# Performance work log

Measured on AMD Instinct MI355X. Metric: run time of the kernel, lower is better.

Reference implementation:

```python
import jax, jax.numpy as jnp
import numpy as np

DIM = 32     # per-head dim in LiteMLA
EPS = 1e-15


def _conv(x, w, groups=1, padding=0, bias=None):
    out = jax.lax.conv_general_dilated(
        x, w, window_strides=(1, 1),
        padding=[(padding, padding), (padding, padding)],
        dimension_numbers=('NCHW', 'OIHW', 'NCHW'),
        feature_group_count=groups)
    if bias is not None:
        out = out + bias[None, :, None, None]
    return out


def _bn(x, g, b):
    # inference-mode BatchNorm2d with running_mean=0, running_var=1
    return x * g[None, :, None, None] + b[None, :, None, None]


def _hswish(x):
    return x * jnp.clip(x + 3.0, 0.0, 6.0) * (1.0 / 6.0)


def _relu_linear_att(kv, q):
    # kv: (B, h*2*DIM, H, W), q: (B, h*DIM, H, W)
    B, _, H, W = kv.shape
    kvr = kv.reshape(B, -1, 2 * DIM, H * W).transpose(0, 1, 3, 2)  # (B,h,HW,2d)
    qr = q.reshape(B, -1, DIM, H * W).transpose(0, 1, 3, 2)        # (B,h,HW,d)
    k = jax.nn.relu(kvr[..., :DIM])
    v = kvr[..., DIM:]
    qf = jax.nn.relu(qr)
    # pad v with a ones column (denominator trick)
    vpad = jnp.pad(v, ((0, 0), (0, 0), (0, 0), (0, 1)), constant_values=1.0)
    ctx = jnp.einsum('bhnd,bhne->bhde', k, vpad)   # (B,h,d,d+1)
    out = jnp.einsum('bhnd,bhde->bhne', qf, ctx)   # (B,h,HW,d+1)
    out = out[..., :-1] / (out[..., -1:] + EPS)
    return out.transpose(0, 1, 3, 2).reshape(B, -1, H, W)


def setup_inputs() -> dict:
    key = jax.random.key(0)
    ks = iter(jax.random.split(key, 40))
    C, B, H, W = 256, 4, 64, 64
    heads = C // DIM  # 8; total_dim = heads*DIM = C

    def rn(shape, s=0.05):
        return jax.random.normal(next(ks), shape, jnp.float32) * s

    inp = {
        'rgb': jax.random.normal(next(ks), (B, C, H, W), jnp.float32),
        't': jax.random.normal(next(ks), (B, C, H, W), jnp.float32),
        # MBConv1: in=2C, mid=round(2C*0.5)=C, out=C, all bn2d, hswish/hswish/None
        'm1_inv_w': rn((C, 2 * C, 1, 1)), 'm1_inv_g': 1.0 + rn((C,)), 'm1_inv_b': rn((C,)),
        'm1_dw_w': rn((C, 1, 3, 3)), 'm1_dw_g': 1.0 + rn((C,)), 'm1_dw_b': rn((C,)),
        'm1_pw_w': rn((C, C, 1, 1)), 'm1_pw_g': 1.0 + rn((C,)), 'm1_pw_b': rn((C,)),
        # LiteMLA projections (1x1, no bias/norm/act)
        'kv_w': rn((4 * C, C, 1, 1)),
        'qrgb_w': rn((C, C, 1, 1)),
        'qt_w': rn((C, C, 1, 1)),
        # multi-scale aggregation (scale=5): depthwise 5x5 then grouped 1x1
        'agg_kv_dw': rn((4 * C, 1, 5, 5)), 'agg_kv_pw': rn((4 * C, DIM, 1, 1)),  # groups=4*heads
        'agg_t_dw': rn((C, 1, 5, 5)), 'agg_t_pw': rn((C, DIM, 1, 1)),            # groups=heads
        'agg_rgb_dw': rn((C, 1, 5, 5)), 'agg_rgb_pw': rn((C, DIM, 1, 1)),
        # proj: 1x1, 2*total_dim*(1+len(scales)) = 4C -> C, no bias, norm 'hswish' unregistered -> None
        'proj_w': rn((C, 4 * C, 1, 1)),
        # MBConv2: mid=4C, use_bias=(T,T,F), norm=(None,None,bn2d), act=(hswish,hswish,None)
        'm2_inv_w': rn((4 * C, C, 1, 1)), 'm2_inv_bias': rn((4 * C,)),
        'm2_dw_w': rn((4 * C, 1, 3, 3)), 'm2_dw_bias': rn((4 * C,)),
        'm2_pw_w': rn((C, 4 * C, 1, 1)), 'm2_pw_g': 1.0 + rn((C,)), 'm2_pw_b': rn((C,)),
    }
    return inp


def reference(rgb, t, m1_inv_w, m1_inv_g, m1_inv_b, m1_dw_w, m1_dw_g, m1_dw_b,
              m1_pw_w, m1_pw_g, m1_pw_b, kv_w, qrgb_w, qt_w,
              agg_kv_dw, agg_kv_pw, agg_t_dw, agg_t_pw, agg_rgb_dw, agg_rgb_pw,
              proj_w, m2_inv_w, m2_inv_bias, m2_dw_w, m2_dw_bias,
              m2_pw_w, m2_pw_g, m2_pw_b):
    C = rgb.shape[1]
    heads = C // DIM
    # MBConv1 on cat(rgb, t)
    x = jnp.concatenate([rgb, t], axis=1)
    x = _hswish(_bn(_conv(x, m1_inv_w), m1_inv_g, m1_inv_b))
    x = _hswish(_bn(_conv(x, m1_dw_w, groups=C, padding=1), m1_dw_g, m1_dw_b))
    rgbt = _bn(_conv(x, m1_pw_w), m1_pw_g, m1_pw_b)
    # LiteMLA
    kv = _conv(rgbt, kv_w)          # (B,4C,H,W)
    q_t = _conv(t, qt_w)            # (B,C,H,W)
    q_rgb = _conv(rgb, qrgb_w)
    kv_s = _conv(_conv(kv, agg_kv_dw, groups=4 * C, padding=2), agg_kv_pw, groups=4 * heads)
    qt_s = _conv(_conv(q_t, agg_t_dw, groups=C, padding=2), agg_t_pw, groups=heads)
    qrgb_s = _conv(_conv(q_rgb, agg_rgb_dw, groups=C, padding=2), agg_rgb_pw, groups=heads)
    kv1 = jnp.concatenate([kv[:, :2 * C], kv_s[:, :2 * C]], axis=1)   # (B,4C,H,W)
    kv2 = jnp.concatenate([kv[:, 2 * C:], kv_s[:, 2 * C:]], axis=1)
    mq_t = jnp.concatenate([q_t, qt_s], axis=1)                       # (B,2C,H,W)
    mq_rgb = jnp.concatenate([q_rgb, qrgb_s], axis=1)
    out1 = _relu_linear_att(kv1, mq_t)
    out2 = _relu_linear_att(kv2, mq_rgb)
    out = _conv(jnp.concatenate([out1, out2], axis=1), proj_w)        # (B,C,H,W)
    # MBConv2
    x = _hswish(_conv(out, m2_inv_w, bias=m2_inv_bias))
    x = _hswish(_conv(x, m2_dw_w, groups=4 * C, padding=1, bias=m2_dw_bias))
    x = _bn(_conv(x, m2_pw_w), m2_pw_g, m2_pw_b)
    return x
```

## Files before the change

kernel.cpp:

```cpp
#include <hip/hip_runtime.h>

#define HW 4096
#define S_E ((size_t)4 * 256 * 4096)

using f16   = _Float16;
using f16x8 = __attribute__((ext_vector_type(8))) _Float16;
using f32x4 = __attribute__((ext_vector_type(4))) float;

__device__ __forceinline__ float hswish(float x) {
  float r = fminf(fmaxf(x + 3.0f, 0.0f), 6.0f);
  return x * r * (1.0f / 6.0f);
}

__device__ __forceinline__ void atomic_add_f32(float* p, float v) {
  __hip_atomic_fetch_add(p, v, __ATOMIC_RELAXED, __HIP_MEMORY_SCOPE_AGENT);
}

__global__ __launch_bounds__(256) void zero_buf4(float4* __restrict__ p, int n4) {
  int i = blockIdx.x * 256 + threadIdx.x;
  if (i < n4) p[i] = make_float4(0.f, 0.f, 0.f, 0.f);
}

__global__ __launch_bounds__(256) void cvt_planes(
    const float* __restrict__ in, f16* __restrict__ hi, f16* __restrict__ lo, int n4)
{
  int i = blockIdx.x * 256 + threadIdx.x;
  if (i >= n4) return;
  float4 v = ((const float4*)in)[i];
  const float* f = &v.x;
  unsigned int hw[2], lw[2];
  #pragma unroll
  for (int j = 0; j < 2; ++j) {
    f16 h0 = (f16)f[2 * j], h1 = (f16)f[2 * j + 1];
    f16 l0 = (f16)(f[2 * j] - (float)h0), l1 = (f16)(f[2 * j + 1] - (float)h1);
    hw[j] = (unsigned int)__builtin_bit_cast(unsigned short, h0) |
            ((unsigned int)__builtin_bit_cast(unsigned short, h1) << 16);
    lw[j] = (unsigned int)__builtin_bit_cast(unsigned short, l0) |
            ((unsigned int)__builtin_bit_cast(unsigned short, l1) << 16);
  }
  *(uint2*)(hi + 4 * (size_t)i) = make_uint2(hw[0], hw[1]);
  *(uint2*)(lo + 4 * (size_t)i) = make_uint2(lw[0], lw[1]);
}

__global__ __launch_bounds__(256) void gemm_mfma(
    const f16* __restrict__ xhi0, const f16* __restrict__ xlo0,
    const f16* __restrict__ xhi1, const f16* __restrict__ xlo1,
    const f16* __restrict__ whi, const f16* __restrict__ wlo,
    float* __restrict__ out, f16* __restrict__ ohi, f16* __restrict__ olo,
    const float* __restrict__ scale, const float* __restrict__ bias,
    int K, int k0, int CO, int epi)
{
  __shared__ f16 Bh[64 * 36];
  __shared__ f16 Bl[64 * 36];
  const int p0  = blockIdx.x * 64;
  const int co0 = blockIdx.y * 128;
  const int b   = blockIdx.z;
  const int tid = threadIdx.x;
  const int lane = tid & 63;
  const int wave = tid >> 6;
  const int wc = wave & 1, wp = wave >> 1;
  const int k1 = K - k0;

  const int tt    = tid & 127;
  const int kbase = (tt >> 3) * 2;
  const int poct  = (tt & 7) * 8;
  const f16* x0 = (tid < 128) ? xhi0 : xlo0;
  const f16* x1 = (tid < 128) ? xhi1 : xlo1;
  f16* Bp = (tid < 128) ? Bh : Bl;

  const int q  = lane >> 4;
  const int ln = lane & 15;

  f32x4 acc[4][2];
  #pragma unroll
  for (int im = 0; im < 4; ++im)
    #pragma unroll
    for (int in = 0; in < 2; ++in)
      acc[im][in] = (f32x4){0.f, 0.f, 0.f, 0.f};

  uint4 g0, g1;
  {
    int kg = kbase;
    const f16* x = (kg < k0) ? x0 + ((size_t)b * k0 + kg) * HW
                             : x1 + ((size_t)b * k1 + (kg - k0)) * HW;
    g0 = *(const uint4*)(x + p0 + poct);
    g1 = *(const uint4*)(x + HW + p0 + poct);
  }

  for (int kt = 0; kt < K; kt += 32) {
    {
      const unsigned short* u0 = (const unsigned short*)&g0;
      const unsigned short* u1 = (const unsigned short*)&g1;
      #pragma unroll
      for (int i = 0; i < 8; ++i) {
        unsigned int d = (unsigned int)u0[i] | ((unsigned int)u1[i] << 16);
        *(unsigned int*)(Bp + (poct + i) * 36 + kbase) = d;
      }
    }
    __syncthreads();
    if (kt + 32 < K) {
      int kg = kt + 32 + kbase;
      const f16* x = (kg < k0) ? x0 + ((size_t)b * k0 + kg) * HW
                               : x1 + ((size_t)b * k1 + (kg - k0)) * HW;
      g0 = *(const uint4*)(x + p0 + poct);
      g1 = *(const uint4*)(x + HW + p0 + poct);
    }
    f16x8 bh[2], bl[2];
    #pragma unroll
    for (int in = 0; in < 2; ++in) {
      const f16* fp = &Bh[(wp * 32 + in * 16 + ln) * 36 + q * 8];
      const f16* gp = &Bl[(wp * 32 + in * 16 + ln) * 36 + q * 8];
      ((uint2*)&bh[in])[0] = *(const uint2*)fp;
      ((uint2*)&bh[in])[1] = *(const uint2*)(fp + 4);
      ((uint2*)&bl[in])[0] = *(const uint2*)gp;
      ((uint2*)&bl[in])[1] = *(const uint2*)(gp + 4);
    }
    #pragma unroll
    for (int im = 0; im < 4; ++im) {
      size_t wofs = (size_t)(co0 + wc * 64 + im * 16 + ln) * K + kt + q * 8;
      f16x8 ah = *(const f16x8*)(whi + wofs);
      f16x8 al = *(const f16x8*)(wlo + wofs);
      #pragma unroll
      for (int in = 0; in < 2; ++in) {
        acc[im][in] = __builtin_amdgcn_mfma_f32_16x16x32_f16(ah, bh[in], acc[im][in], 0, 0, 0);
        acc[im][in] = __builtin_amdgcn_mfma_f32_16x16x32_f16(ah, bl[in], acc[im][in], 0, 0, 0);
        acc[im][in] = __builtin_amdgcn_mfma_f32_16x16x32_f16(al, bh[in], acc[im][in], 0, 0, 0);
      }
    }
    __syncthreads();
  }

  #pragma unroll
  for (int im = 0; im < 4; ++im) {
    #pragma unroll
    for (int in = 0; in < 2; ++in) {
      int p = p0 + wp * 32 + in * 16 + ln;
      #pragma unroll
      for (int r = 0; r < 4; ++r) {
        int co = co0 + wc * 64 + im * 16 + q * 4 + r;
        float v = acc[im][in][r];
        if (epi == 1)      v = v * scale[co] + bias[co];
        else if (epi == 2) v = hswish(v * scale[co] + bias[co]);
        else if (epi == 3) v = hswish(v + bias[co]);
        size_t idx = ((size_t)b * CO + co) * HW + p;
        if (out) out[idx] = v;
        else {
          f16 h = (f16)v;
          ohi[idx] = h;
          olo[idx] = (f16)(v - (float)h);
        }
      }
    }
  }
}

__global__ __launch_bounds__(256) void dwconv3(
    const float* __restrict__ in, const float* __restrict__ w,
    float* __restrict__ out, f16* __restrict__ ohi, f16* __restrict__ olo,
    const float* __restrict__ scale, const float* __restrict__ bias,
    int Cmask, int epi, int pmode)
{
  __shared__ float tl[66 * 66];
  const int bc = blockIdx.x;
  const int c  = bc & Cmask;
  const float* src = in + (size_t)bc * HW;
  const int t = threadIdx.x;
  for (int i = t; i < 66 * 66; i += 256) {
    int r = i / 66, cc = i - r * 66;
    int gy = r - 1, gx = cc - 1;
    float v = 0.0f;
    if (gy >= 0 && gy < 64 && gx >= 0 && gx < 64) v = src[(gy << 6) + gx];
    tl[i] = v;
  }
  const float* wp = w + c * 9;
  float w00 = wp[0], w01 = wp[1], w02 = wp[2];
  float w10 = wp[3], w11 = wp[4], w12 = wp[5];
  float w20 = wp[6], w21 = wp[7], w22 = wp[8];
  float g = (epi == 2) ? scale[c] : 1.0f;
  float bb = bias[c];
  __syncthreads();
  #pragma unroll 4
  for (int j = 0; j < 16; ++j) {
    int p = j * 256 + t;
    int y = p >> 6, x = p & 63;
    const float* bp = &tl[y * 66 + x];
    float s;
    s = w00 * bp[0]        + w01 * bp[1]        + w02 * bp[2];
    s = fmaf(w10, bp[66],    fmaf(w11, bp[67],    fmaf(w12, bp[68],  s)));
    s = fmaf(w20, bp[132],   fmaf(w21, bp[133],   fmaf(w22, bp[134], s)));
    float v = (epi == 2) ? hswish(s * g + bb) : hswish(s + bb);
    size_t idx = (size_t)bc * HW + p;
    if (pmode) {
      f16 h = (f16)v;
      ohi[idx] = h;
      olo[idx] = (f16)(v - (float)h);
    } else {
      out[idx] = v;
    }
  }
}

__global__ __launch_bounds__(256) void agg_fused(
    const float* __restrict__ in, const float* __restrict__ dw,
    const float* __restrict__ pw, float* __restrict__ out, int C)
{
  __shared__ float in_t[16 * 12 * 68];
  __shared__ float dww[32 * 25];
  __shared__ float pww[32 * 32];
  const int g = blockIdx.x, b = blockIdx.y, tile = blockIdx.z;
  const int t = threadIdx.x;
  const int y0 = tile * 8;
  const float* src = in + ((size_t)b * C + g * 32) * HW;

  for (int i = t; i < 800; i += 256)  dww[i] = dw[(size_t)g * 800 + i];
  for (int i = t; i < 1024; i += 256) pww[i] = pw[(size_t)g * 1024 + i];

  const int x = t & 63, yl = t >> 6;
  float acca[32] = {}, accb[32] = {};

  for (int ph = 0; ph < 2; ++ph) {
    __syncthreads();
    #pragma unroll
    for (int i = 0; i < 12; ++i) {
      int id = i * 256 + t;
      int qq = id & 15;
      int rid = id >> 4;
      int ch = rid / 12, r = rid - ch * 12;
      int gy = y0 - 2 + r;
      float4 v = make_float4(0.f, 0.f, 0.f, 0.f);
      if (gy >= 0 && gy < 64)
        v = *(const float4*)(src + (size_t)(ph * 16 + ch) * HW + (gy << 6) + (qq << 2));
      *(float4*)&in_t[(ch * 12 + r) * 68 + 2 + (qq << 2)] = v;
    }
    #pragma unroll
    for (int i = 0; i < 3; ++i) {
      int id = i * 256 + t;
      int side = id & 3;
      int rid = id >> 2;
      int col = (side < 2) ? side : 64 + side;
      in_t[rid * 68 + col] = 0.0f;
    }
    __syncthreads();
    for (int cl = 0; cl < 16; ++cl) {
      int ci = ph * 16 + cl;
      const float* bp = &in_t[(cl * 12) * 68 + 2 + x];
      const float* wv = &dww[ci * 25];
      float da = 0.f, db = 0.f;
      #pragma unroll
      for (int k = 0; k < 25; ++k) {
        int dy = k / 5, dx = (k % 5) - 2;
        float w = wv[k];
        da = fmaf(w, bp[(yl + dy) * 68 + dx], da);
        db = fmaf(w, bp[(yl + 4 + dy) * 68 + dx], db);
      }
      #pragma unroll
      for (int m = 0; m < 32; ++m) {
        float w = pww[m * 32 + ci];
        acca[m] = fmaf(w, da, acca[m]);
        accb[m] = fmaf(w, db, accb[m]);
      }
    }
  }
  float* dst = out + ((size_t)b * C + g * 32) * HW + y0 * 64;
  #pragma unroll
  for (int m = 0; m < 32; ++m) {
    dst[(size_t)m * HW + (yl << 6) + x]        = acca[m];
    dst[(size_t)m * HW + ((yl + 4) << 6) + x]  = accb[m];
  }
}

__global__ __launch_bounds__(256) void att_ctx(
    const float* __restrict__ kv, const float* __restrict__ kvs,
    float* __restrict__ ctxbuf)
{
  __shared__ float tile[64 * 128];
  __shared__ float red[4 * 1056];
  const int head  = blockIdx.x;
  const int b     = blockIdx.y;
  const int slice = blockIdx.z & 31;
  const int z     = blockIdx.z >> 5;
  const int tid   = threadIdx.x;
  const int lane  = tid & 63;
  const int wave  = tid >> 6;
  const int td = lane & 7, te = lane >> 3;

  const float* kvsrc = (head < 8)
      ? kv  + ((size_t)b * 1024 + z * 512 + head * 64) * HW
      : kvs + ((size_t)b * 1024 + z * 512 + (head - 8) * 64) * HW;
  const int n0 = slice * 128;

  #pragma unroll
  for (int j = 0; j < 8; ++j) {
    int slot = j * 256 + tid;
    int ch = slot >> 5;
    int nb = slot & 31;
    float4 v = *(const float4*)(kvsrc + (size_t)ch * HW + n0 + (nb << 2));
    if (ch < 32) {
      v.x = fmaxf(v.x, 0.0f); v.y = fmaxf(v.y, 0.0f);
      v.z = fmaxf(v.z, 0.0f); v.w = fmaxf(v.w, 0.0f);
    }
    int sw = nb ^ ((ch >> 2) & 7);
    *(float4*)&tile[ch * 128 + (sw << 2)] = v;
  }
  __syncthreads();

  float acc[4][4] = {};
  float cs[4] = {};
  #pragma unroll
  for (int j = 0; j < 8; ++j) {
    int nblk = wave * 8 + j;
    float4 kr[4], vr[4];
    #pragma unroll
    for (int r = 0; r < 4; ++r) {
      int d = td * 4 + r;
      kr[r] = *(const float4*)&tile[d * 128 + ((nblk ^ td) << 2)];
      int e = 32 + te * 4 + r;
      vr[r] = *(const float4*)&tile[e * 128 + ((nblk ^ te) << 2)];
    }
    #pragma unroll
    for (int r = 0; r < 4; ++r) {
      const float* kp = &kr[r].x;
      cs[r] += kp[0] + kp[1] + kp[2] + kp[3];
      #pragma unroll
      for (int rp = 0; rp < 4; ++rp) {
        const float* vp = &vr[rp].x;
        acc[r][rp] = fmaf(kp[0], vp[0],
                     fmaf(kp[1], vp[1],
                     fmaf(kp[2], vp[2],
                     fmaf(kp[3], vp[3], acc[r][rp]))));
      }
    }
  }

  float* rw = &red[wave * 1056];
  #pragma unroll
  for (int r = 0; r < 4; ++r) {
    #pragma unroll
    for (int rp = 0; rp < 4; ++rp)
      rw[(td * 4 + r) * 33 + te * 4 + rp] = acc[r][rp];
    if (te == 0) rw[(td * 4 + r) * 33 + 32] = cs[r];
  }
  __syncthreads();

  float* cp = ctxbuf + (size_t)(((z * 4 + b) * 16) + head) * 1056;
  for (int i = tid; i < 1056; i += 256) {
    float s = red[i] + red[1056 + i] + red[2112 + i] + red[3168 + i];
    atomic_add_f32(cp + i, s);
  }
}

__global__ __launch_bounds__(256) void att_apply(
    const float* __restrict__ ctxbuf,
    const float* __restrict__ q0, const float* __restrict__ q0s,
    const float* __restrict__ q1, const float* __restrict__ q1s,
    f16* __restrict__ H)
{
  __shared__ float ctx[1056];
  const int head = blockIdx.x;
  const int b    = blockIdx.y;
  const int tile = blockIdx.z & 15;
  const int z    = blockIdx.z >> 4;
  const int tid  = threadIdx.x;

  const float* cp = ctxbuf + (size_t)(((z * 4 + b) * 16) + head) * 1056;
  for (int i = tid; i < 1056; i += 256) ctx[i] = cp[i];
  __syncthreads();

  const float* qb = (z == 0) ? (head < 8 ? q0 : q0s) : (head < 8 ? q1 : q1s);
  const float* qsrc = qb + ((size_t)b * 256 + (head & 7) * 32) * HW;
  f16* oh = H + (size_t)z * (4 * S_E);
  f16* ol = oh + 2 * S_E;

  const int n = tile * 256 + tid;
  float qv[32];
  #pragma unroll
  for (int d = 0; d < 32; ++d)
    qv[d] = fmaxf(qsrc[(size_t)d * HW + n], 0.0f);
  float den = 1e-15f;
  #pragma unroll
  for (int d = 0; d < 32; ++d)
    den = fmaf(qv[d], ctx[d * 33 + 32], den);
  float rden = 1.0f / den;
  for (int e = 0; e < 32; ++e) {
    float s = 0.0f;
    #pragma unroll
    for (int d = 0; d < 32; ++d)
      s = fmaf(qv[d], ctx[d * 33 + e], s);
    float v = s * rden;
    size_t idx = ((size_t)b * 512 + head * 32 + e) * HW + n;
    f16 h = (f16)v;
    oh[idx] = h;
    ol[idx] = (f16)(v - (float)h);
  }
}

extern "C" void kernel_launch(void* const* d_in, const int* in_sizes, int n_in,
                              void* d_out, int out_size, void* d_ws, size_t ws_size,
                              hipStream_t stream) {
  (void)in_sizes; (void)n_in; (void)out_size; (void)ws_size;
  const float* rgb         = (const float*)d_in[0];
  const float* t           = (const float*)d_in[1];
  const float* m1_inv_w    = (const float*)d_in[2];
  const float* m1_inv_g    = (const float*)d_in[3];
  const float* m1_inv_b    = (const float*)d_in[4];
  const float* m1_dw_w     = (const float*)d_in[5];
  const float* m1_dw_g     = (const float*)d_in[6];
  const float* m1_dw_b     = (const float*)d_in[7];
  const float* m1_pw_w     = (const float*)d_in[8];
  const float* m1_pw_g     = (const float*)d_in[9];
  const float* m1_pw_b     = (const float*)d_in[10];
  const float* kv_w        = (const float*)d_in[11];
  const float* qrgb_w      = (const float*)d_in[12];
  const float* qt_w        = (const float*)d_in[13];
  const float* agg_kv_dw   = (const float*)d_in[14];
  const float* agg_kv_pw   = (const float*)d_in[15];
  const float* agg_t_dw    = (const float*)d_in[16];
  const float* agg_t_pw    = (const float*)d_in[17];
  const float* agg_rgb_dw  = (const float*)d_in[18];
  const float* agg_rgb_pw  = (const float*)d_in[19];
  const float* proj_w      = (const float*)d_in[20];
  const float* m2_inv_w    = (const float*)d_in[21];
  const float* m2_inv_bias = (const float*)d_in[22];
  const float* m2_dw_w     = (const float*)d_in[23];
  const float* m2_dw_bias  = (const float*)d_in[24];
  const float* m2_pw_w     = (const float*)d_in[25];
  const float* m2_pw_g     = (const float*)d_in[26];
  const float* m2_pw_b     = (const float*)d_in[27];
  float* outp = (float*)d_out;

  const size_t S = S_E;
  float* ws = (float*)d_ws;
  f16*   rgbH  = (f16*)(ws + 0 * S);
  f16*   tH    = (f16*)(ws + 1 * S);
  float* s2    = ws + 2 * S;
  f16*   dw1H  = (f16*)(ws + 3 * S);
  float* s3f   = ws + 3 * S;
  f16*   rgbtH = (f16*)(ws + 4 * S);
  float* s4f   = ws + 4 * S;
  float* s5    = ws + 5 * S;
  float* KV    = ws + 6 * S;
  f16*   attH  = (f16*)(ws + 6 * S);
  float* KVS   = ws + 10 * S;
  float* CTX   = ws + 14 * S;
  float* WB    = ws + 14 * S + 150016;
  f16*   projH = (f16*)(ws + 15 * S);

  f16* wb = (f16*)WB;
  f16* w_m1inv = wb;
  f16* w_m1pw  = wb + 262144;
  f16* w_kv    = wb + 393216;
  f16* w_qt    = wb + 917504;
  f16* w_qrgb  = wb + 1048576;
  f16* w_proj  = wb + 1179648;
  f16* w_m2inv = wb + 1703936;
  f16* w_m2pw  = wb + 2228224;

  dim3 blk(256);
  const int XN4 = (int)(S_E / 4);

  cvt_planes<<<dim3(4096), blk, 0, stream>>>(rgb, rgbH, rgbH + S_E, XN4);
  cvt_planes<<<dim3(4096), blk, 0, stream>>>(t,   tH,   tH   + S_E, XN4);
  cvt_planes<<<dim3(128), blk, 0, stream>>>(m1_inv_w, w_m1inv, w_m1inv + 131072, 32768);
  cvt_planes<<<dim3(64),  blk, 0, stream>>>(m1_pw_w,  w_m1pw,  w_m1pw  + 65536, 16384);
  cvt_planes<<<dim3(256), blk, 0, stream>>>(kv_w,     w_kv,    w_kv    + 262144, 65536);
  cvt_planes<<<dim3(64),  blk, 0, stream>>>(qt_w,     w_qt,    w_qt    + 65536, 16384);
  cvt_planes<<<dim3(64),  blk, 0, stream>>>(qrgb_w,   w_qrgb,  w_qrgb  + 65536, 16384);
  cvt_planes<<<dim3(256), blk, 0, stream>>>(proj_w,   w_proj,  w_proj  + 262144, 65536);
  cvt_planes<<<dim3(256), blk, 0, stream>>>(m2_inv_w, w_m2inv, w_m2inv + 262144, 65536);
  cvt_planes<<<dim3(256), blk, 0, stream>>>(m2_pw_w,  w_m2pw,  w_m2pw  + 262144, 65536);

  gemm_mfma<<<dim3(64, 2, 4), blk, 0, stream>>>(
      rgbH, rgbH + S_E, tH, tH + S_E, w_m1inv, w_m1inv + 131072,
      s2, nullptr, nullptr, m1_inv_g, m1_inv_b, 512, 256, 256, 2);
  dwconv3<<<dim3(1024), blk, 0, stream>>>(
      s2, m1_dw_w, nullptr, dw1H, dw1H + S_E, m1_dw_g, m1_dw_b, 255, 2, 1);
  gemm_mfma<<<dim3(64, 2, 4), blk, 0, stream>>>(
      dw1H, dw1H + S_E, dw1H, dw1H + S_E, w_m1pw, w_m1pw + 65536,
      nullptr, rgbtH, rgbtH + S_E, m1_pw_g, m1_pw_b, 256, 256, 256, 1);

  gemm_mfma<<<dim3(64, 8, 4), blk, 0, stream>>>(
      rgbtH, rgbtH + S_E, rgbtH, rgbtH + S_E, w_kv, w_kv + 262144,
      KV, nullptr, nullptr, nullptr, nullptr, 256, 256, 1024, 0);
  gemm_mfma<<<dim3(64, 2, 4), blk, 0, stream>>>(
      tH, tH + S_E, tH, tH + S_E, w_qt, w_qt + 65536,
      s2, nullptr, nullptr, nullptr, nullptr, 256, 256, 256, 0);
  gemm_mfma<<<dim3(64, 2, 4), blk, 0, stream>>>(
      rgbH, rgbH + S_E, rgbH, rgbH + S_E, w_qrgb, w_qrgb + 65536,
      s5, nullptr, nullptr, nullptr, nullptr, 256, 256, 256, 0);

  agg_fused<<<dim3(32, 4, 8), blk, 0, stream>>>(KV, agg_kv_dw, agg_kv_pw, KVS, 1024);
  agg_fused<<<dim3(8, 4, 8),  blk, 0, stream>>>(s2, agg_t_dw,  agg_t_pw,  s3f, 256);
  agg_fused<<<dim3(8, 4, 8),  blk, 0, stream>>>(s5, agg_rgb_dw, agg_rgb_pw, s4f, 256);

  zero_buf4<<<dim3(132), blk, 0, stream>>>((float4*)CTX, 128 * 264);
  att_ctx<<<dim3(16, 4, 64), blk, 0, stream>>>(KV, KVS, CTX);
  att_apply<<<dim3(16, 4, 32), blk, 0, stream>>>(CTX, s2, s3f, s5, s4f, attH);

  gemm_mfma<<<dim3(64, 2, 4), blk, 0, stream>>>(
      attH, attH + 2 * S_E, attH + 4 * S_E, attH + 6 * S_E, w_proj, w_proj + 262144,
      nullptr, projH, projH + S_E, nullptr, nullptr, 1024, 512, 256, 0);
  gemm_mfma<<<dim3(64, 8, 4), blk, 0, stream>>>(
      projH, projH + S_E, projH, projH + S_E, w_m2inv, w_m2inv + 262144,
      KVS, nullptr, nullptr, nullptr, m2_inv_bias, 256, 256, 1024, 3);
  dwconv3<<<dim3(4096), blk, 0, stream>>>(
      KVS, m2_dw_w, nullptr, (f16*)(ws + 6 * S), (f16*)(ws + 8 * S),
      nullptr, m2_dw_bias, 1023, 3, 1);
  gemm_mfma<<<dim3(64, 2, 4), blk, 0, stream>>>(
      (f16*)(ws + 6 * S), (f16*)(ws + 8 * S), (f16*)(ws + 6 * S), (f16*)(ws + 8 * S),
      w_m2pw, w_m2pw + 262144,
      outp, nullptr, nullptr, m2_pw_g, m2_pw_b, 1024, 1024, 256, 1);
}
```

Baseline: 845.2 us.

## Double-buffer LDS tiles in MFMA GEMM with two-stage global prefetch

New measurement: 885.5 us. 1.05x slower.

```diff
diff --git a/kernel.cpp b/kernel.cpp
--- a/kernel.cpp
+++ b/kernel.cpp
@@ -6,6 +6,8 @@
 using f16   = _Float16;
 using f16x8 = __attribute__((ext_vector_type(8))) _Float16;
 using f32x4 = __attribute__((ext_vector_type(4))) float;
+
+template<int N> struct IC { static constexpr int v = N; };
 
 __device__ __forceinline__ float hswish(float x) {
   float r = fminf(fmaxf(x + 3.0f, 0.0f), 6.0f);
@@ -50,8 +52,8 @@
     const float* __restrict__ scale, const float* __restrict__ bias,
     int K, int k0, int CO, int epi)
 {
-  __shared__ f16 Bh[64 * 36];
-  __shared__ f16 Bl[64 * 36];
+  __shared__ f16 Bh[2][64 * 36];
+  __shared__ f16 Bl[2][64 * 36];
   const int p0  = blockIdx.x * 64;
   const int co0 = blockIdx.y * 128;
   const int b   = blockIdx.z;
@@ -66,7 +68,8 @@
   const int poct  = (tt & 7) * 8;
   const f16* x0 = (tid < 128) ? xhi0 : xlo0;
   const f16* x1 = (tid < 128) ? xhi1 : xlo1;
-  f16* Bp = (tid < 128) ? Bh : Bl;
+  f16* Bp0 = (tid < 128) ? Bh[0] : Bl[0];
+  f16* Bp1 = (tid < 128) ? Bh[1] : Bl[1];
 
   const int q  = lane >> 4;
   const int ln = lane & 15;
@@ -78,56 +81,91 @@
     for (int in = 0; in < 2; ++in)
       acc[im][in] = (f32x4){0.f, 0.f, 0.f, 0.f};
 
-  uint4 g0, g1;
+  auto gaddr = [&](int kg) -> const f16* {
+    return (kg < k0) ? x0 + ((size_t)b * k0 + kg) * HW
+                     : x1 + ((size_t)b * k1 + (kg - k0)) * HW;
+  };
+
+  uint4 gA0, gA1, gB0, gB1;
   {
-    int kg = kbase;
-    const f16* x = (kg < k0) ? x0 + ((size_t)b * k0 + kg) * HW
-                             : x1 + ((size_t)b * k1 + (kg - k0)) * HW;
-    g0 = *(const uint4*)(x + p0 + poct);
-    g1 = *(const uint4*)(x + HW + p0 + poct);
-  }
-
-  for (int kt = 0; kt < K; kt += 32) {
-    {
-      const unsigned short* u0 = (const unsigned short*)&g0;
-      const unsigned short* u1 = (const unsigned short*)&g1;
-      #pragma unroll
-      for (int i = 0; i < 8; ++i) {
-        unsigned int d = (unsigned int)u0[i] | ((unsigned int)u1[i] << 16);
-        *(unsigned int*)(Bp + (poct + i) * 36 + kbase) = d;
-      }
-    }
-    __syncthreads();
-    if (kt + 32 < K) {
-      int kg = kt + 32 + kbase;
-      const f16* x = (kg < k0) ? x0 + ((size_t)b * k0 + kg) * HW
-                               : x1 + ((size_t)b * k1 + (kg - k0)) * HW;
-      g0 = *(const uint4*)(x + p0 + poct);
-      g1 = *(const uint4*)(x + HW + p0 + poct);
+    const f16* x = gaddr(kbase);
+    gA0 = *(const uint4*)(x + p0 + poct);
+    gA1 = *(const uint4*)(x + HW + p0 + poct);
+  }
+  {
+    const unsigned short* u0 = (const unsigned short*)&gA0;
+    const unsigned short* u1 = (const unsigned short*)&gA1;
+    #pragma unroll
+    for (int i = 0; i < 8; ++i) {
+      unsigned int d = (unsigned int)u0[i] | ((unsigned int)u1[i] << 16);
+      *(unsigned int*)(Bp0 + (poct + i) * 36 + kbase) = d;
+    }
+  }
+  {
+    const f16* x = gaddr(32 + kbase);
+    gB0 = *(const uint4*)(x + p0 + poct);
+    gB1 = *(const uint4*)(x + HW + p0 + poct);
+  }
+  __builtin_amdgcn_sched_barrier(0);
+  asm volatile("s_waitcnt lgkmcnt(0)" ::: "memory");
+  __builtin_amdgcn_s_barrier();
+  __builtin_amdgcn_sched_barrier(0);
+
+  auto subiter = [&](auto Sc, int kt) {
+    constexpr int S = decltype(Sc)::v;
+    const int kk = kt + S * 32;
+    f16x8 wh[4], wl[4];
+    #pragma unroll
+    for (int im = 0; im < 4; ++im) {
+      size_t wofs = (size_t)(co0 + wc * 64 + im * 16 + ln) * K + kk + q * 8;
+      wh[im] = *(const f16x8*)(whi + wofs);
+      wl[im] = *(const f16x8*)(wlo + wofs);
     }
     f16x8 bh[2], bl[2];
     #pragma unroll
     for (int in = 0; in < 2; ++in) {
-      const f16* fp = &Bh[(wp * 32 + in * 16 + ln) * 36 + q * 8];
-      const f16* gp = &Bl[(wp * 32 + in * 16 + ln) * 36 + q * 8];
+      const f16* fp = &Bh[S][(wp * 32 + in * 16 + ln) * 36 + q * 8];
+      const f16* gp = &Bl[S][(wp * 32 + in * 16 + ln) * 36 + q * 8];
       ((uint2*)&bh[in])[0] = *(const uint2*)fp;
       ((uint2*)&bh[in])[1] = *(const uint2*)(fp + 4);
       ((uint2*)&bl[in])[0] = *(const uint2*)gp;
       ((uint2*)&bl[in])[1] = *(const uint2*)(gp + 4);
     }
+    if (kk + 64 < K) {
+      const f16* x = gaddr(kk + 64 + kbase);
+      if (S) { gB0 = *(const uint4*)(x + p0 + poct); gB1 = *(const uint4*)(x + HW + p0 + poct); }
+      else   { gA0 = *(const uint4*)(x + p0 + poct); gA1 = *(const uint4*)(x + HW + p0 + poct); }
+    }
     #pragma unroll
     for (int im = 0; im < 4; ++im) {
-      size_t wofs = (size_t)(co0 + wc * 64 + im * 16 + ln) * K + kt + q * 8;
-      f16x8 ah = *(const f16x8*)(whi + wofs);
-      f16x8 al = *(const f16x8*)(wlo + wofs);
       #pragma unroll
       for (int in = 0; in < 2; ++in) {
-        acc[im][in] = __builtin_amdgcn_mfma_f32_16x16x32_f16(ah, bh[in], acc[im][in], 0, 0, 0);
-        acc[im][in] = __builtin_amdgcn_mfma_f32_16x16x32_f16(ah, bl[in], acc[im][in], 0, 0, 0);
-        acc[im][in] = __builtin_amdgcn_mfma_f32_16x16x32_f16(al, bh[in], acc[im][in], 0, 0, 0);
+        acc[im][in] = __builtin_amdgcn_mfma_f32_16x16x32_f16(wh[im], bh[in], acc[im][in], 0, 0, 0);
+        acc[im][in] = __builtin_amdgcn_mfma_f32_16x16x32_f16(wh[im], bl[in], acc[im][in], 0, 0, 0);
+        acc[im][in] = __builtin_amdgcn_mfma_f32_16x16x32_f16(wl[im], bh[in], acc[im][in], 0, 0, 0);
       }
     }
-    __syncthreads();
+    if (kk + 32 < K) {
+      f16* Bw = S ? Bp0 : Bp1;
+      const uint4 h0 = S ? gA0 : gB0;
+      const uint4 h1 = S ? gA1 : gB1;
+      const unsigned short* u0 = (const unsigned short*)&h0;
+      const unsigned short* u1 = (const unsigned short*)&h1;
+      #pragma unroll
+      for (int i = 0; i < 8; ++i) {
+        unsigned int d = (unsigned int)u0[i] | ((unsigned int)u1[i] << 16);
+        *(unsigned int*)(Bw + (poct + i) * 36 + kbase) = d;
+      }
+      __builtin_amdgcn_sched_barrier(0);
+      asm volatile("s_waitcnt lgkmcnt(0)" ::: "memory");
+      __builtin_amdgcn_s_barrier();
+      __builtin_amdgcn_sched_barrier(0);
+    }
+  };
+
+  for (int kt = 0; kt < K; kt += 64) {
+    subiter(IC<0>{}, kt);
+    subiter(IC<1>{}, kt);
   }
 
   #pragma unroll
```

## Emit transposed packed hi/lo activations and stream them directly into MFMA GEMMs

Applied to the files above, without the earlier changes.

New measurement: 912.5 us. +8.0%, slower.

```diff
diff --git a/kernel.cpp b/kernel.cpp
--- a/kernel.cpp
+++ b/kernel.cpp
@@ -6,6 +6,7 @@
 using f16   = _Float16;
 using f16x8 = __attribute__((ext_vector_type(8))) _Float16;
 using f32x4 = __attribute__((ext_vector_type(4))) float;
+using u32x4 = __attribute__((ext_vector_type(4))) unsigned int;
 
 __device__ __forceinline__ float hswish(float x) {
   float r = fminf(fmaxf(x + 3.0f, 0.0f), 6.0f);
@@ -47,6 +48,7 @@
     const f16* __restrict__ xhi1, const f16* __restrict__ xlo1,
     const f16* __restrict__ whi, const f16* __restrict__ wlo,
     float* __restrict__ out, f16* __restrict__ ohi, f16* __restrict__ olo,
+    unsigned int* __restrict__ oxt,
     const float* __restrict__ scale, const float* __restrict__ bias,
     int K, int k0, int CO, int epi)
 {
@@ -135,6 +137,119 @@
     #pragma unroll
     for (int in = 0; in < 2; ++in) {
       int p = p0 + wp * 32 + in * 16 + ln;
+      if (oxt) {
+        unsigned int pk[4];
+        #pragma unroll
+        for (int r = 0; r < 4; ++r) {
+          int co = co0 + wc * 64 + im * 16 + q * 4 + r;
+          float v = acc[im][in][r];
+          if (epi == 1)      v = v * scale[co] + bias[co];
+          else if (epi == 2) v = hswish(v * scale[co] + bias[co]);
+          else if (epi == 3) v = hswish(v + bias[co]);
+          f16 h = (f16)v;
+          f16 l = (f16)(v - (float)h);
+          pk[r] = ((unsigned int)__builtin_bit_cast(unsigned short, h) << 16) |
+                   (unsigned int)__builtin_bit_cast(unsigned short, l);
+        }
+        int cob = co0 + wc * 64 + im * 16 + q * 4;
+        *(uint4*)(oxt + ((size_t)b * HW + p) * CO + cob) =
+            make_uint4(pk[0], pk[1], pk[2], pk[3]);
+      } else {
+        #pragma unroll
+        for (int r = 0; r < 4; ++r) {
+          int co = co0 + wc * 64 + im * 16 + q * 4 + r;
+          float v = acc[im][in][r];
+          if (epi == 1)      v = v * scale[co] + bias[co];
+          else if (epi == 2) v = hswish(v * scale[co] + bias[co]);
+          else if (epi == 3) v = hswish(v + bias[co]);
+          size_t idx = ((size_t)b * CO + co) * HW + p;
+          if (out) out[idx] = v;
+          else {
+            f16 h = (f16)v;
+            ohi[idx] = h;
+            olo[idx] = (f16)(v - (float)h);
+          }
+        }
+      }
+    }
+  }
+}
+
+__global__ __launch_bounds__(256) void gemm_stream(
+    const unsigned int* __restrict__ XT,
+    const f16* __restrict__ whi, const f16* __restrict__ wlo,
+    float* __restrict__ out,
+    const float* __restrict__ scale, const float* __restrict__ bias,
+    int K, int CO, int epi)
+{
+  const int p0  = blockIdx.x * 64;
+  const int co0 = blockIdx.y * 128;
+  const int b   = blockIdx.z;
+  const int tid = threadIdx.x;
+  const int lane = tid & 63;
+  const int wave = tid >> 6;
+  const int wc = wave & 1, wp = wave >> 1;
+  const int q  = lane >> 4;
+  const int ln = lane & 15;
+
+  const unsigned int* xb = XT + (size_t)b * HW * K;
+
+  f32x4 acc[4][2];
+  #pragma unroll
+  for (int im = 0; im < 4; ++im)
+    #pragma unroll
+    for (int in = 0; in < 2; ++in)
+      acc[im][in] = (f32x4){0.f, 0.f, 0.f, 0.f};
+
+  #pragma unroll 2
+  for (int kt = 0; kt < K; kt += 32) {
+    u32x4 a[2], c[2];
+    #pragma unroll
+    for (int in = 0; in < 2; ++in) {
+      int p = p0 + wp * 32 + in * 16 + ln;
+      const unsigned int* src = xb + (size_t)p * K + kt + q * 8;
+      a[in] = *(const u32x4*)src;
+      c[in] = *(const u32x4*)(src + 4);
+    }
+    f16x8 wh[4], wl[4];
+    #pragma unroll
+    for (int im = 0; im < 4; ++im) {
+      size_t wofs = (size_t)(co0 + wc * 64 + im * 16 + ln) * K + kt + q * 8;
+      wh[im] = *(const f16x8*)(whi + wofs);
+      wl[im] = *(const f16x8*)(wlo + wofs);
+    }
+    f16x8 bh[2], bl[2];
+    #pragma unroll
+    for (int in = 0; in < 2; ++in) {
+      u32x4 hh, ll;
+      hh.x = (a[in].x >> 16) | (a[in].y & 0xffff0000u);
+      hh.y = (a[in].z >> 16) | (a[in].w & 0xffff0000u);
+      hh.z = (c[in].x >> 16) | (c[in].y & 0xffff0000u);
+      hh.w = (c[in].z >> 16) | (c[in].w & 0xffff0000u);
+      ll.x = (a[in].x & 0xffffu) | (a[in].y << 16);
+      ll.y = (a[in].z & 0xffffu) | (a[in].w << 16);
+      ll.z = (c[in].x & 0xffffu) | (c[in].w << 16 & 0u) | (c[in].w << 16);
+      ll.z = (c[in].x & 0xffffu) | (c[in].y << 16);
+      ll.w = (c[in].z & 0xffffu) | (c[in].w << 16);
+      bh[in] = __builtin_bit_cast(f16x8, hh);
+      bl[in] = __builtin_bit_cast(f16x8, ll);
+    }
+    #pragma unroll
+    for (int im = 0; im < 4; ++im) {
+      #pragma unroll
+      for (int in = 0; in < 2; ++in) {
+        acc[im][in] = __builtin_amdgcn_mfma_f32_16x16x32_f16(wh[im], bh[in], acc[im][in], 0, 0, 0);
+        acc[im][in] = __builtin_amdgcn_mfma_f32_16x16x32_f16(wh[im], bl[in], acc[im][in], 0, 0, 0);
+        acc[im][in] = __builtin_amdgcn_mfma_f32_16x16x32_f16(wl[im], bh[in], acc[im][in], 0, 0, 0);
+      }
+    }
+  }
+
+  #pragma unroll
+  for (int im = 0; im < 4; ++im) {
+    #pragma unroll
+    for (int in = 0; in < 2; ++in) {
+      int p = p0 + wp * 32 + in * 16 + ln;
       #pragma unroll
       for (int r = 0; r < 4; ++r) {
         int co = co0 + wc * 64 + im * 16 + q * 4 + r;
@@ -142,13 +257,7 @@
         if (epi == 1)      v = v * scale[co] + bias[co];
         else if (epi == 2) v = hswish(v * scale[co] + bias[co]);
         else if (epi == 3) v = hswish(v + bias[co]);
-        size_t idx = ((size_t)b * CO + co) * HW + p;
-        if (out) out[idx] = v;
-        else {
-          f16 h = (f16)v;
-          ohi[idx] = h;
-          olo[idx] = (f16)(v - (float)h);
-        }
+        out[((size_t)b * CO + co) * HW + p] = v;
       }
     }
   }
@@ -435,7 +544,7 @@
   float* s2    = ws + 2 * S;
   f16*   dw1H  = (f16*)(ws + 3 * S);
   float* s3f   = ws + 3 * S;
-  f16*   rgbtH = (f16*)(ws + 4 * S);
+  unsigned int* XT_rgbt = (unsigned int*)(ws + 4 * S);
   float* s4f   = ws + 4 * S;
   float* s5    = ws + 5 * S;
   float* KV    = ws + 6 * S;
@@ -443,7 +552,7 @@
   float* KVS   = ws + 10 * S;
   float* CTX   = ws + 14 * S;
   float* WB    = ws + 14 * S + 150016;
-  f16*   projH = (f16*)(ws + 15 * S);
+  unsigned int* XT_proj = (unsigned int*)(ws + 15 * S);
 
   f16* wb = (f16*)WB;
   f16* w_m1inv = wb;
@@ -471,22 +580,21 @@
 
   gemm_mfma<<<dim3(64, 2, 4), blk, 0, stream>>>(
       rgbH, rgbH + S_E, tH, tH + S_E, w_m1inv, w_m1inv + 131072,
-      s2, nullptr, nullptr, m1_inv_g, m1_inv_b, 512, 256, 256, 2);
+      s2, nullptr, nullptr, nullptr, m1_inv_g, m1_inv_b, 512, 256, 256, 2);
   dwconv3<<<dim3(1024), blk, 0, stream>>>(
       s2, m1_dw_w, nullptr, dw1H, dw1H + S_E, m1_dw_g, m1_dw_b, 255, 2, 1);
   gemm_mfma<<<dim3(64, 2, 4), blk, 0, stream>>>(
       dw1H, dw1H + S_E, dw1H, dw1H + S_E, w_m1pw, w_m1pw + 65536,
-      nullptr, rgbtH, rgbtH + S_E, m1_pw_g, m1_pw_b, 256, 256, 256, 1);
-
-  gemm_mfma<<<dim3(64, 8, 4), blk, 0, stream>>>(
-      rgbtH, rgbtH + S_E, rgbtH, rgbtH + S_E, w_kv, w_kv + 262144,
-      KV, nullptr, nullptr, nullptr, nullptr, 256, 256, 1024, 0);
+      nullptr, nullptr, nullptr, XT_rgbt, m1_pw_g, m1_pw_b, 256, 256, 256, 1);
+
+  gemm_stream<<<dim3(64, 8, 4), blk, 0, stream>>>(
+      XT_rgbt, w_kv, w_kv + 262144, KV, nullptr, nullptr, 256, 1024, 0);
   gemm_mfma<<<dim3(64, 2, 4), blk, 0, stream>>>(
       tH, tH + S_E, tH, tH + S_E, w_qt, w_qt + 65536,
-      s2, nullptr, nullptr, nullptr, nullptr, 256, 256, 256, 0);
+      s2, nullptr, nullptr, nullptr, nullptr, nullptr, 256, 256, 256, 0);
   gemm_mfma<<<dim3(64, 2, 4), blk, 0, stream>>>(
       rgbH, rgbH + S_E, rgbH, rgbH + S_E, w_qrgb, w_qrgb + 65536,
-      s5, nullptr, nullptr, nullptr, nullptr, 256, 256, 256, 0);
+      s5, nullptr, nullptr, nullptr, nullptr, nullptr, 256, 256, 256, 0);
 
   agg_fused<<<dim3(32, 4, 8), blk, 0, stream>>>(KV, agg_kv_dw, agg_kv_pw, KVS, 1024);
   agg_fused<<<dim3(8, 4, 8),  blk, 0, stream>>>(s2, agg_t_dw,  agg_t_pw,  s3f, 256);
@@ -498,15 +606,14 @@
 
   gemm_mfma<<<dim3(64, 2, 4), blk, 0, stream>>>(
       attH, attH + 2 * S_E, attH + 4 * S_E, attH + 6 * S_E, w_proj, w_proj + 262144,
-      nullptr, projH, projH + S_E, nullptr, nullptr, 1024, 512, 256, 0);
-  gemm_mfma<<<dim3(64, 8, 4), blk, 0, stream>>>(
-      projH, projH + S_E, projH, projH + S_E, w_m2inv, w_m2inv + 262144,
-      KVS, nullptr, nullptr, nullptr, m2_inv_bias, 256, 256, 1024, 3);
+      nullptr, nullptr, nullptr, XT_proj, nullptr, nullptr, 1024, 512, 256, 0);
+  gemm_stream<<<dim3(64, 8, 4), blk, 0, stream>>>(
+      XT_proj, w_m2inv, w_m2inv + 262144, KVS, nullptr, m2_inv_bias, 256, 1024, 3);
   dwconv3<<<dim3(4096), blk, 0, stream>>>(
       KVS, m2_dw_w, nullptr, (f16*)(ws + 6 * S), (f16*)(ws + 8 * S),
       nullptr, m2_dw_bias, 1023, 3, 1);
   gemm_mfma<<<dim3(64, 2, 4), blk, 0, stream>>>(
       (f16*)(ws + 6 * S), (f16*)(ws + 8 * S), (f16*)(ws + 6 * S), (f16*)(ws + 8 * S),
       w_m2pw, w_m2pw + 262144,
-      outp, nullptr, nullptr, m2_pw_g, m2_pw_b, 1024, 1024, 256, 1);
-}
+      outp, nullptr, nullptr, nullptr, m2_pw_g, m2_pw_b, 1024, 1024, 256, 1);
+}
```
